# Kernel tuning notes

Measured on AMD Instinct MI355X. Metric: run time of the kernel, lower is better.

Reference implementation:

```python
import jax, jax.numpy as jnp
import numpy as np

M, NQ, NK, DX, H, HD, DT, KH = 2, 1024, 1024, 512, 8, 64, 2, 32
SCALE = HD ** -0.5


def setup_inputs() -> dict:
    key = jax.random.key(0)
    ks = jax.random.split(key, 12)
    w = lambda k, shape: jax.random.normal(k, shape, jnp.float32) * 0.02
    return dict(
        xq=jax.random.normal(ks[0], (M, NQ, DX), jnp.float32),
        xk=jax.random.normal(ks[1], (M, NK, DX), jnp.float32),
        xv=jax.random.normal(ks[2], (M, NK, DX), jnp.float32),
        tq=jax.random.normal(ks[3], (M, NQ, DT), jnp.float32),
        tk=jax.random.normal(ks[4], (M, NK, DT), jnp.float32),
        Wq=w(ks[5], (DX, H * HD)),
        Wk=w(ks[6], (DX, H * HD)),
        Wv=w(ks[7], (DX, H * HD)),
        Wo=w(ks[8], (H * HD, DX)),
        bo=jnp.zeros((DX,), jnp.float32),
        K1=w(ks[9], (DT, KH)),
        kb1=jnp.zeros((KH,), jnp.float32),
        K2=w(ks[10], (KH, H)),
        kb2=jnp.zeros((H,), jnp.float32),
    )


def _heads(t):
    # [b, n, h*d] -> [b, h, n, d]
    b, n, _ = t.shape
    return t.reshape(b, n, H, HD).transpose(0, 2, 1, 3)


def reference(xq, xk, xv, tq, tk, Wq, Wk, Wv, Wo, bo, K1, kb1, K2, kb2):
    q = _heads(xq @ Wq)            # [m,h,nq,d]
    k = _heads(xk @ Wk)            # [m,h,nk,d]
    token_dots = jnp.einsum('bhqd,bhkd->bhqk', q, k) * SCALE
    # diagonal attention term: query attends to its own (key/value-projected) token
    xq_k = _heads(xq @ Wk)
    diag_dots = jnp.sum(q * xq_k, axis=-1, keepdims=True) * SCALE   # [m,h,nq,1]
    token_dots = jnp.concatenate([token_dots, diag_dots], axis=-1)  # [m,h,nq,nk+1]
    # translation group action: pairwise differences, plus zero diagonal diff
    diff = tq[:, :, None, :] - tk[:, None, :, :]                    # [m,nq,nk,dt]
    diff = jnp.concatenate([diff, jnp.zeros((M, NQ, 1, DT), diff.dtype)], axis=2)
    # kernel network (MLP) -> per-head relative-position bias [m,nq,nk+1,h]
    kd = jax.nn.relu(diff @ K1 + kb1) @ K2 + kb2
    dots = token_dots + kd.transpose(0, 3, 1, 2)                    # [m,h,nq,nk+1]
    attn = jax.nn.softmax(dots, axis=-1)
    v = _heads(xv @ Wv)
    xq_v = _heads(xq @ Wv)
    out = jnp.einsum('bhqk,bhkd->bhqd', attn[..., :-1], v) + attn[..., -1:] * xq_v
    out = out.transpose(0, 2, 1, 3).reshape(M, NQ, H * HD) @ Wo + bo
    # phi_t is None -> tq_new = tq
    return (out, tq)
```

## Files before the change

kernel.cpp:

```cpp
#include <hip/hip_runtime.h>
#include <hip/hip_bf16.h>
#include <cstddef>

typedef __attribute__((ext_vector_type(8))) short bf16x8;
typedef __attribute__((ext_vector_type(4))) float f32x4;

constexpr int NH  = 8;
constexpr int HHD = 512;
constexpr int KHC = 32;
constexpr float SCALE_F = 0.125f;
constexpr int KSPLIT = 2;

__device__ __forceinline__ unsigned short f2bf(float f) {
    unsigned int u = __builtin_bit_cast(unsigned int, f);
    u = (u + 0x7FFFu + ((u >> 16) & 1u)) >> 16;
    return (unsigned short)u;
}
__device__ __forceinline__ float bf2f(unsigned short h) {
    unsigned int u = ((unsigned int)h) << 16;
    return __builtin_bit_cast(float, u);
}
__device__ __forceinline__ unsigned int cvt_pk_bf16(float lo, float hi) {
    unsigned int r;
    asm("v_cvt_pk_bf16_f32 %0, %1, %2" : "=v"(r) : "v"(lo), "v"(hi));
    return r;
}

struct Cast3 { const float* s[3]; unsigned short* d[3]; };
__global__ __launch_bounds__(256) void cast_x(Cast3 c) {
    const int z = blockIdx.z;
    const size_t i8 = ((size_t)blockIdx.x * 256 + threadIdx.x) * 8;
    const float4 f0 = *(const float4*)(c.s[z] + i8);
    const float4 f1 = *(const float4*)(c.s[z] + i8 + 4);
    ushort4 o0, o1;
    o0.x = f2bf(f0.x); o0.y = f2bf(f0.y); o0.z = f2bf(f0.z); o0.w = f2bf(f0.w);
    o1.x = f2bf(f1.x); o1.y = f2bf(f1.y); o1.z = f2bf(f1.z); o1.w = f2bf(f1.w);
    *(ushort4*)(c.d[z] + i8) = o0;
    *(ushort4*)(c.d[z] + i8 + 4) = o1;
}

struct Cast4 { const float* s[4]; unsigned short* d[4]; };
__global__ __launch_bounds__(256) void cast_wt(Cast4 c) {
    __shared__ unsigned short Ts[64][66];
    const int z = blockIdx.z;
    const float* W = c.s[z];
    unsigned short* Wt = c.d[z];
    const int t = threadIdx.x;
    const int k0 = blockIdx.x * 64, j0 = blockIdx.y * 64;

    {
        const int kr = t >> 2;
        const int jc = (t & 3) * 16;
        const float* g = W + (size_t)(k0 + kr) * 512 + j0 + jc;
        #pragma unroll
        for (int i4 = 0; i4 < 4; ++i4) {
            float4 f = *(const float4*)(g + i4 * 4);
            Ts[kr][jc + i4 * 4 + 0] = f2bf(f.x);
            Ts[kr][jc + i4 * 4 + 1] = f2bf(f.y);
            Ts[kr][jc + i4 * 4 + 2] = f2bf(f.z);
            Ts[kr][jc + i4 * 4 + 3] = f2bf(f.w);
        }
    }
    __syncthreads();
    {
        const int j = t >> 2;
        const int kseg = (t & 3) * 16;
        unsigned short tmp[16];
        #pragma unroll
        for (int i = 0; i < 16; ++i) tmp[i] = Ts[kseg + i][j];
        unsigned short* g = Wt + (size_t)(j0 + j) * 512 + k0 + kseg;
        #pragma unroll
        for (int i4 = 0; i4 < 4; ++i4)
            *(ushort4*)(g + i4 * 4) = *(ushort4*)&tmp[i4 * 4];
    }
}

__device__ __forceinline__ void mfma_gemm_core(const unsigned short* __restrict__ A,
                                               const unsigned short* __restrict__ Bt,
                                               int r0, int c0, f32x4 acc[2][4])
{
    __shared__ __align__(16) char As[16384];
    __shared__ __align__(16) char Bs[8192];

    const int tid = threadIdx.x;
    const int l = tid & 63, w = tid >> 6;
    const int lw = l & 15, lg = l >> 4;

    #pragma unroll
    for (int r = 0; r < 2; ++r)
        #pragma unroll
        for (int cb = 0; cb < 4; ++cb) acc[r][cb] = (f32x4){0.f, 0.f, 0.f, 0.f};

    const int arow_s = tid >> 1;
    const int ahalf  = tid & 1;
    const int brow_s = tid >> 2;
    const int bseg   = tid & 3;

    for (int kb = 0; kb < 512; kb += 64) {
        __syncthreads();
        {
            const unsigned short* g = A + (size_t)(r0 + arow_s) * 512 + kb + ahalf * 32;
            const int base = arow_s * 128 + ahalf * 64;
            const int sw = (arow_s & 7) << 4;
            #pragma unroll
            for (int i = 0; i < 4; ++i)
                *(float4*)(As + ((base + i * 16) ^ sw)) = *(const float4*)(g + i * 8);
        }
        {
            const unsigned short* g = Bt + (size_t)(c0 + brow_s) * 512 + kb + bseg * 16;
            const int base = brow_s * 128 + bseg * 32;
            const int sw = (brow_s & 7) << 4;
            #pragma unroll
            for (int i = 0; i < 2; ++i)
                *(float4*)(Bs + ((base + i * 16) ^ sw)) = *(const float4*)(g + i * 8);
        }
        __syncthreads();

        bf16x8 bfrag[4][2];
        #pragma unroll
        for (int cb = 0; cb < 4; ++cb) {
            const int bcol = cb * 16 + lw;
            const int sw = (bcol & 7) << 4;
            bfrag[cb][0] = *(const bf16x8*)(Bs + ((bcol * 128 + lg * 16) ^ sw));
            bfrag[cb][1] = *(const bf16x8*)(Bs + ((bcol * 128 + 64 + lg * 16) ^ sw));
        }
        #pragma unroll
        for (int r = 0; r < 2; ++r) {
            const int arow = w * 32 + r * 16 + lw;
            const int sw = (arow & 7) << 4;
            bf16x8 a0 = *(const bf16x8*)(As + ((arow * 128 + lg * 16) ^ sw));
            bf16x8 a1 = *(const bf16x8*)(As + ((arow * 128 + 64 + lg * 16) ^ sw));
            #pragma unroll
            for (int cb = 0; cb < 4; ++cb) {
                acc[r][cb] = __builtin_amdgcn_mfma_f32_16x16x32_bf16(a0, bfrag[cb][0], acc[r][cb], 0, 0, 0);
                acc[r][cb] = __builtin_amdgcn_mfma_f32_16x16x32_bf16(a1, bfrag[cb][1], acc[r][cb], 0, 0, 0);
            }
        }
    }
}

struct Proj5 {
    const unsigned short* A[5];
    const unsigned short* B[5];
    unsigned short* O[5];
    unsigned short* VT;
};

__global__ __launch_bounds__(256) void proj_mfma(Proj5 p) {
    const int z = blockIdx.z;
    const int r0 = blockIdx.x * 128, c0 = blockIdx.y * 64;
    f32x4 acc[2][4];
    mfma_gemm_core(p.A[z], p.B[z], r0, c0, acc);

    const int l = threadIdx.x & 63, w = threadIdx.x >> 6;
    const int lw = l & 15, lg = l >> 4;
    #pragma unroll
    for (int r = 0; r < 2; ++r)
        #pragma unroll
        for (int cb = 0; cb < 4; ++cb) {
            const int gc = c0 + cb * 16 + lw;
            const int h = gc >> 6, d = gc & 63;
            #pragma unroll
            for (int rr = 0; rr < 4; ++rr) {
                const int gr = r0 + w * 32 + r * 16 + lg * 4 + rr;
                const int m = gr >> 10, n = gr & 1023;
                const unsigned short v = f2bf(acc[r][cb][rr]);
                if (z == 2)
                    p.VT[(((size_t)m * NH + h) * 64 + d) * 1024 + n] = v;
                else
                    p.O[z][(((size_t)m * NH + h) * 1024 + n) * 64 + d] = v;
            }
        }
}

__global__ __launch_bounds__(256) void outproj_mfma(const unsigned short* __restrict__ A,
                                                    const unsigned short* __restrict__ Bt,
                                                    const float* __restrict__ bias,
                                                    float* __restrict__ C) {
    const int r0 = blockIdx.x * 128, c0 = blockIdx.y * 64;
    f32x4 acc[2][4];
    mfma_gemm_core(A, Bt, r0, c0, acc);

    const int l = threadIdx.x & 63, w = threadIdx.x >> 6;
    const int lw = l & 15, lg = l >> 4;
    #pragma unroll
    for (int r = 0; r < 2; ++r)
        #pragma unroll
        for (int cb = 0; cb < 4; ++cb) {
            const int gc = c0 + cb * 16 + lw;
            const float bv = bias[gc];
            #pragma unroll
            for (int rr = 0; rr < 4; ++rr) {
                const int gr = r0 + w * 32 + r * 16 + lg * 4 + rr;
                C[(size_t)gr * HHD + gc] = acc[r][cb][rr] + bv;
            }
        }
}

__global__ __launch_bounds__(256) void prep_k(const float* __restrict__ tq,
                                              const float* __restrict__ tk,
                                              const float* __restrict__ K1,
                                              const float* __restrict__ kb1,
                                              float* __restrict__ Aout,
                                              float* __restrict__ Bout)
{
    const int idx = blockIdx.x * 256 + threadIdx.x;
    const int which = idx >> 16;
    const int e = idx & 65535;
    const int row = e >> 5;
    const int j = e & 31;
    const float* t = which ? tk : tq;
    float v = t[row * 2 + 0] * K1[j] + t[row * 2 + 1] * K1[KHC + j];
    if (!which) v += kb1[j];
    (which ? Bout : Aout)[e] = v;
}

__global__ __launch_bounds__(256) void bias_mfma(const float* __restrict__ Aa,
                                                 const float* __restrict__ Bb,
                                                 const float* __restrict__ K2,
                                                 const float* __restrict__ kb2,
                                                 unsigned short* __restrict__ kd)
{
    const int tid = threadIdx.x;
    const int l = tid & 63;
    const int kb = tid >> 6;
    const int lw = l & 15, lg = l >> 4;
    const int bid = blockIdx.x;
    const int kt = bid & 15;
    const int qg = (bid >> 4) & 63;
    const int m  = bid >> 10;

    float k2f[8];
    #pragma unroll
    for (int e = 0; e < 8; ++e)
        k2f[e] = (lw < 8) ? K2[(lg * 8 + e) * 8 + lw] : 0.f;
    union { unsigned int u[4]; bf16x8 v; } bu;
    #pragma unroll
    for (int i = 0; i < 4; ++i) bu.u[i] = cvt_pk_bf16(k2f[2 * i], k2f[2 * i + 1]);
    const bf16x8 bfrag = bu.v;

    const float c0 = (lw < 8) ? kb2[lw] : 0.f;
    const f32x4 cini = {c0, c0, c0, c0};

    const int kglob = kt * 64 + kb * 16 + lw;
    const float* bp = Bb + ((size_t)m * 1024 + kglob) * 32 + lg * 8;
    const float4 b0 = *(const float4*)bp;
    const float4 b1 = *(const float4*)(bp + 4);
    const float bl[8] = {b0.x, b0.y, b0.z, b0.w, b1.x, b1.y, b1.z, b1.w};

    const float* arow = Aa + ((size_t)m * 1024 + qg * 16) * 32 + lg * 8;
    unsigned short* kout = kd + (size_t)(m * 8 + lw) * 1048576
                         + qg * 16384 + kt * 1024 + kb * 256 + lg * 64;

    #pragma unroll
    for (int t = 0; t < 16; t += 2) {
        const float4 a00 = *(const float4*)(arow + (size_t)t * 32);
        const float4 a01 = *(const float4*)(arow + (size_t)t * 32 + 4);
        union { unsigned int u[4]; bf16x8 v; } r0u;
        r0u.u[0] = cvt_pk_bf16(fmaxf(a00.x - bl[0], 0.f), fmaxf(a00.y - bl[1], 0.f));
        r0u.u[1] = cvt_pk_bf16(fmaxf(a00.z - bl[2], 0.f), fmaxf(a00.w - bl[3], 0.f));
        r0u.u[2] = cvt_pk_bf16(fmaxf(a01.x - bl[4], 0.f), fmaxf(a01.y - bl[5], 0.f));
        r0u.u[3] = cvt_pk_bf16(fmaxf(a01.z - bl[6], 0.f), fmaxf(a01.w - bl[7], 0.f));
        const f32x4 d0 = __builtin_amdgcn_mfma_f32_16x16x32_bf16(r0u.v, bfrag, cini, 0, 0, 0);

        const float4 a10 = *(const float4*)(arow + (size_t)(t + 1) * 32);
        const float4 a11 = *(const float4*)(arow + (size_t)(t + 1) * 32 + 4);
        union { unsigned int u[4]; bf16x8 v; } r1u;
        r1u.u[0] = cvt_pk_bf16(fmaxf(a10.x - bl[0], 0.f), fmaxf(a10.y - bl[1], 0.f));
        r1u.u[1] = cvt_pk_bf16(fmaxf(a10.z - bl[2], 0.f), fmaxf(a10.w - bl[3], 0.f));
        r1u.u[2] = cvt_pk_bf16(fmaxf(a11.x - bl[4], 0.f), fmaxf(a11.y - bl[5], 0.f));
        r1u.u[3] = cvt_pk_bf16(fmaxf(a11.z - bl[6], 0.f), fmaxf(a11.w - bl[7], 0.f));
        const f32x4 d1 = __builtin_amdgcn_mfma_f32_16x16x32_bf16(r1u.v, bfrag, cini, 0, 0, 0);

        if (lw < 8) {
            uint4 o;
            o.x = cvt_pk_bf16(d0[0], d0[1]);
            o.y = cvt_pk_bf16(d0[2], d0[3]);
            o.z = cvt_pk_bf16(d1[0], d1[1]);
            o.w = cvt_pk_bf16(d1[2], d1[3]);
            *(uint4*)(kout + t * 4) = o;
        }
    }
}

__global__ __launch_bounds__(256) void attn_mfma(
    const unsigned short* __restrict__ qh, const unsigned short* __restrict__ kh,
    const unsigned short* __restrict__ vt, const unsigned short* __restrict__ kd,
    float* __restrict__ pacc, float* __restrict__ pl)
{
    __shared__ __align__(16) char Ksh[8192];
    __shared__ __align__(16) char Vsh[8192];
    __shared__ __align__(16) char Psh[4][2048];

    const int tid = threadIdx.x;
    const int l = tid & 63;
    const int w = tid >> 6;
    const int lw = l & 15, lg = l >> 4;
    const int qt = blockIdx.x;
    const int mh = blockIdx.y;
    const int ks = blockIdx.z;
    const int q0 = qt * 64;

    const int qrow = q0 + w * 16 + lw;
    const unsigned short* qp = qh + ((size_t)mh * 1024 + qrow) * 64;
    const bf16x8 qf0 = *(const bf16x8*)(qp + lg * 8);
    const bf16x8 qf1 = *(const bf16x8*)(qp + 32 + lg * 8);

    f32x4 oacc[4] = {{0.f,0.f,0.f,0.f},{0.f,0.f,0.f,0.f},
                     {0.f,0.f,0.f,0.f},{0.f,0.f,0.f,0.f}};
    float lsum = 0.f;

    const int srow = tid >> 2;
    const int scol = (tid & 3) * 32;
    const int ssw  = (srow & 7) << 4;

    char* pbase = Psh[w];
    const int prsw = (lw & 7) << 4;
    const size_t kdwave = (((size_t)mh * 64 + qt * 4 + w) * 16 + ks * 8) * 1024;

    for (int kt = 0; kt < 8; ++kt) {
        const int k0 = ks * 512 + kt * 64;
        __syncthreads();
        {
            const char* g = (const char*)(kh + ((size_t)mh * 1024 + k0 + srow) * 64) + scol;
            const int a = srow * 128 + scol;
            *(float4*)(Ksh + (a ^ ssw))        = *(const float4*)g;
            *(float4*)(Ksh + ((a + 16) ^ ssw)) = *(const float4*)(g + 16);
        }
        {
            const char* g = (const char*)(vt + ((size_t)mh * 64 + srow) * 1024 + k0) + scol;
            const int a = srow * 128 + scol;
            *(float4*)(Vsh + (a ^ ssw))        = *(const float4*)g;
            *(float4*)(Vsh + ((a + 16) ^ ssw)) = *(const float4*)(g + 16);
        }
        __syncthreads();

        const unsigned short* kdt = kd + kdwave + (size_t)kt * 1024;
        #pragma unroll
        for (int kb = 0; kb < 4; ++kb) {
            f32x4 s = {0.f, 0.f, 0.f, 0.f};
            const int row = kb * 16 + lw;
            const int rsw = (row & 7) << 4;
            const int a0 = row * 128 + lg * 16;
            bf16x8 af0 = *(const bf16x8*)(Ksh + (a0 ^ rsw));
            s = __builtin_amdgcn_mfma_f32_16x16x32_bf16(af0, qf0, s, 0, 0, 0);
            bf16x8 af1 = *(const bf16x8*)(Ksh + ((a0 + 64) ^ rsw));
            s = __builtin_amdgcn_mfma_f32_16x16x32_bf16(af1, qf1, s, 0, 0, 0);

            ushort4 bb = *(const ushort4*)(kdt + kb * 256 + l * 4);
            float p0 = __expf(fmaf(s[0], SCALE_F, bf2f(bb.x)));
            float p1 = __expf(fmaf(s[1], SCALE_F, bf2f(bb.y)));
            float p2 = __expf(fmaf(s[2], SCALE_F, bf2f(bb.z)));
            float p3 = __expf(fmaf(s[3], SCALE_F, bf2f(bb.w)));
            lsum += (p0 + p1) + (p2 + p3);

            unsigned int u0 = f2bf(p0) | ((unsigned int)f2bf(p1) << 16);
            unsigned int u1 = f2bf(p2) | ((unsigned int)f2bf(p3) << 16);
            const int pa = lw * 128 + kb * 32 + lg * 8;
            *(uint2*)(pbase + (pa ^ prsw)) = make_uint2(u0, u1);
        }

        #pragma unroll
        for (int kc = 0; kc < 2; ++kc) {
            const int pa = lw * 128 + kc * 64 + lg * 16;
            bf16x8 pfrag = *(const bf16x8*)(pbase + (pa ^ prsw));
            #pragma unroll
            for (int db = 0; db < 4; ++db) {
                const int vrow = db * 16 + lw;
                const int va = vrow * 128 + kc * 64 + lg * 16;
                bf16x8 vfrag = *(const bf16x8*)(Vsh + (va ^ ((vrow & 7) << 4)));
                oacc[db] = __builtin_amdgcn_mfma_f32_16x16x32_bf16(pfrag, vfrag, oacc[db], 0, 0, 0);
            }
        }
    }

    lsum += __shfl_xor(lsum, 16, 64);
    lsum += __shfl_xor(lsum, 32, 64);

    float* pr = pacc + (((size_t)mh * KSPLIT + ks) * 1024) * 64;
    #pragma unroll
    for (int r = 0; r < 4; ++r) {
        const int qo = q0 + w * 16 + lg * 4 + r;
        float* rowp = pr + (size_t)qo * 64 + lw;
        rowp[0]  = oacc[0][r];
        rowp[16] = oacc[1][r];
        rowp[32] = oacc[2][r];
        rowp[48] = oacc[3][r];
    }
    if (lg == 0)
        pl[((size_t)mh * KSPLIT + ks) * 1024 + q0 + w * 16 + lw] = lsum;
}

__global__ __launch_bounds__(256) void reduce_k(
    const float* __restrict__ pacc, const float* __restrict__ pl,
    const unsigned short* __restrict__ qg, const unsigned short* __restrict__ xqk,
    const unsigned short* __restrict__ xqv, const float* __restrict__ K2,
    const float* __restrict__ kb1, const float* __restrict__ kb2,
    unsigned short* __restrict__ attn_out)
{
    const int rowid = blockIdx.x * 4 + (threadIdx.x >> 6);
    const int d = threadIdx.x & 63;
    const int mh = rowid >> 10;
    const int q = rowid & 1023;
    const int m = mh >> 3;
    const int h = mh & 7;

    float accsum = 0.f, lsumv = 0.f;
    #pragma unroll
    for (int kc = 0; kc < KSPLIT; ++kc) {
        accsum += pacc[(((size_t)mh * KSPLIT + kc) * 1024 + q) * 64 + d];
        lsumv  += pl[((size_t)mh * KSPLIT + kc) * 1024 + q];
    }
    const size_t ro = ((size_t)mh * 1024 + q) * 64 + d;
    float s = bf2f(qg[ro]) * bf2f(xqk[ro]);
    #pragma unroll
    for (int off = 32; off > 0; off >>= 1) s += __shfl_xor(s, off, 64);
    float bias_d = kb2[h];
    #pragma unroll
    for (int j = 0; j < KHC; ++j) bias_d += fmaxf(kb1[j], 0.f) * K2[j * NH + h];
    const float pd = __expf(fmaf(s, SCALE_F, bias_d));
    const float outv = (accsum + pd * bf2f(xqv[ro])) / (lsumv + pd);
    attn_out[((size_t)(m * 1024 + q)) * HHD + h * 64 + d] = f2bf(outv);
}

extern "C" void kernel_launch(void* const* d_in, const int* in_sizes, int n_in,
                              void* d_out, int out_size, void* d_ws, size_t ws_size,
                              hipStream_t stream)
{
    const float* xq  = (const float*)d_in[0];
    const float* xk  = (const float*)d_in[1];
    const float* xv  = (const float*)d_in[2];
    const float* tq  = (const float*)d_in[3];
    const float* tk  = (const float*)d_in[4];
    const float* Wq  = (const float*)d_in[5];
    const float* Wk  = (const float*)d_in[6];
    const float* Wv  = (const float*)d_in[7];
    const float* Wo  = (const float*)d_in[8];
    const float* bo  = (const float*)d_in[9];
    const float* K1  = (const float*)d_in[10];
    const float* kb1 = (const float*)d_in[11];
    const float* K2  = (const float*)d_in[12];
    const float* kb2 = (const float*)d_in[13];

    char* ws = (char*)d_ws;
    unsigned short* qh   = (unsigned short*)(ws);
    unsigned short* kh   = (unsigned short*)(ws +  2097152);
    unsigned short* vtp  = (unsigned short*)(ws +  4194304);
    unsigned short* xqk  = (unsigned short*)(ws +  6291456);
    unsigned short* xqv  = (unsigned short*)(ws +  8388608);
    float*          Aa   = (float*)(ws + 10485760);
    float*          Bb   = (float*)(ws + 10747904);
    unsigned short* kd   = (unsigned short*)(ws + 11010048);
    float*          pacc = (float*)(ws + 44564480);
    float*          pl   = (float*)(ws + 52953088);
    unsigned short* Wot  = (unsigned short*)(ws + 53084160);
    unsigned short* xa   = (unsigned short*)(ws + 11010048);
    unsigned short* xb   = (unsigned short*)(ws + 13107200);
    unsigned short* xc   = (unsigned short*)(ws + 15204352);
    unsigned short* Wqt  = (unsigned short*)(ws + 17301504);
    unsigned short* Wkt  = (unsigned short*)(ws + 17825792);
    unsigned short* Wvt  = (unsigned short*)(ws + 18350080);
    unsigned short* aout = (unsigned short*)(ws + 11010048);
    float*          outp = (float*)d_out;

    Cast3 c3; c3.s[0] = xq; c3.s[1] = xk; c3.s[2] = xv;
    c3.d[0] = xa; c3.d[1] = xb; c3.d[2] = xc;
    hipLaunchKernelGGL(cast_x, dim3(512, 1, 3), dim3(256), 0, stream, c3);
    Cast4 c4; c4.s[0] = Wq; c4.s[1] = Wk; c4.s[2] = Wv; c4.s[3] = Wo;
    c4.d[0] = Wqt; c4.d[1] = Wkt; c4.d[2] = Wvt; c4.d[3] = Wot;
    hipLaunchKernelGGL(cast_wt, dim3(8, 8, 4), dim3(256), 0, stream, c4);

    Proj5 p;
    p.A[0] = xa; p.B[0] = Wqt; p.O[0] = qh;
    p.A[1] = xb; p.B[1] = Wkt; p.O[1] = kh;
    p.A[2] = xc; p.B[2] = Wvt; p.O[2] = nullptr;
    p.A[3] = xa; p.B[3] = Wkt; p.O[3] = xqk;
    p.A[4] = xa; p.B[4] = Wvt; p.O[4] = xqv;
    p.VT = vtp;
    hipLaunchKernelGGL(proj_mfma, dim3(16, 8, 5), dim3(256), 0, stream, p);

    hipLaunchKernelGGL(prep_k, dim3(512), dim3(256), 0, stream, tq, tk, K1, kb1, Aa, Bb);

    hipLaunchKernelGGL(bias_mfma, dim3(2048), dim3(256), 0, stream, Aa, Bb, K2, kb2, kd);

    hipLaunchKernelGGL(attn_mfma, dim3(16, 16, KSPLIT), dim3(256), 0, stream,
                       qh, kh, vtp, kd, pacc, pl);

    hipLaunchKernelGGL(reduce_k, dim3(4096), dim3(256), 0, stream,
                       pacc, pl, qh, xqk, xqv, K2, kb1, kb2, aout);

    hipLaunchKernelGGL(outproj_mfma, dim3(16, 8, 1), dim3(256), 0, stream, aout, Wot, bo, outp);

    hipMemcpyAsync(outp + 1048576, tq, 4096 * sizeof(float),
                   hipMemcpyDeviceToDevice, stream);
}
```

Baseline: 164.7 us.

## Merge prep kernels into one launch and raise attention key split to four

Folds the three preparation kernels (activation cast, weight cast-transpose, kernel-MLP first layer) into a single launch that dispatches on block index, removing two kernel launches. Raises the attention key-split from 2 to 4 so the attention grid doubles to 1024 blocks with shorter loops, and adds a launch-bounds occupancy hint. The partial-accumulator buffer grows, so the workspace offsets are moved, and the reduction kernel must now combine more partials.

```diff
diff --git a/kernel.cpp b/kernel.cpp
--- a/kernel.cpp
+++ b/kernel.cpp
@@ -9,7 +9,7 @@
 constexpr int HHD = 512;
 constexpr int KHC = 32;
 constexpr float SCALE_F = 0.125f;
-constexpr int KSPLIT = 2;
+constexpr int KSPLIT = 4;
 
 __device__ __forceinline__ unsigned short f2bf(float f) {
     unsigned int u = __builtin_bit_cast(unsigned int, f);
@@ -26,52 +26,70 @@
     return r;
 }
 
-struct Cast3 { const float* s[3]; unsigned short* d[3]; };
-__global__ __launch_bounds__(256) void cast_x(Cast3 c) {
-    const int z = blockIdx.z;
-    const size_t i8 = ((size_t)blockIdx.x * 256 + threadIdx.x) * 8;
-    const float4 f0 = *(const float4*)(c.s[z] + i8);
-    const float4 f1 = *(const float4*)(c.s[z] + i8 + 4);
-    ushort4 o0, o1;
-    o0.x = f2bf(f0.x); o0.y = f2bf(f0.y); o0.z = f2bf(f0.z); o0.w = f2bf(f0.w);
-    o1.x = f2bf(f1.x); o1.y = f2bf(f1.y); o1.z = f2bf(f1.z); o1.w = f2bf(f1.w);
-    *(ushort4*)(c.d[z] + i8) = o0;
-    *(ushort4*)(c.d[z] + i8 + 4) = o1;
-}
-
-struct Cast4 { const float* s[4]; unsigned short* d[4]; };
-__global__ __launch_bounds__(256) void cast_wt(Cast4 c) {
+struct PrepAll {
+    const float* xs[3]; unsigned short* xd[3];
+    const float* wsrc[4]; unsigned short* wdst[4];
+    const float* tq; const float* tk;
+    const float* K1; const float* kb1;
+    float* Aa; float* Bb;
+};
+__global__ __launch_bounds__(256) void prep_all(PrepAll c) {
     __shared__ unsigned short Ts[64][66];
-    const int z = blockIdx.z;
-    const float* W = c.s[z];
-    unsigned short* Wt = c.d[z];
+    const int b = blockIdx.x;
     const int t = threadIdx.x;
-    const int k0 = blockIdx.x * 64, j0 = blockIdx.y * 64;
-
-    {
-        const int kr = t >> 2;
-        const int jc = (t & 3) * 16;
-        const float* g = W + (size_t)(k0 + kr) * 512 + j0 + jc;
-        #pragma unroll
-        for (int i4 = 0; i4 < 4; ++i4) {
-            float4 f = *(const float4*)(g + i4 * 4);
-            Ts[kr][jc + i4 * 4 + 0] = f2bf(f.x);
-            Ts[kr][jc + i4 * 4 + 1] = f2bf(f.y);
-            Ts[kr][jc + i4 * 4 + 2] = f2bf(f.z);
-            Ts[kr][jc + i4 * 4 + 3] = f2bf(f.w);
-        }
-    }
-    __syncthreads();
-    {
-        const int j = t >> 2;
-        const int kseg = (t & 3) * 16;
-        unsigned short tmp[16];
-        #pragma unroll
-        for (int i = 0; i < 16; ++i) tmp[i] = Ts[kseg + i][j];
-        unsigned short* g = Wt + (size_t)(j0 + j) * 512 + k0 + kseg;
-        #pragma unroll
-        for (int i4 = 0; i4 < 4; ++i4)
-            *(ushort4*)(g + i4 * 4) = *(ushort4*)&tmp[i4 * 4];
+
+    if (b < 1536) {
+        const int z = b / 512;
+        const size_t i8 = ((size_t)(b - z * 512) * 256 + t) * 8;
+        const float4 f0 = *(const float4*)(c.xs[z] + i8);
+        const float4 f1 = *(const float4*)(c.xs[z] + i8 + 4);
+        ushort4 o0, o1;
+        o0.x = f2bf(f0.x); o0.y = f2bf(f0.y); o0.z = f2bf(f0.z); o0.w = f2bf(f0.w);
+        o1.x = f2bf(f1.x); o1.y = f2bf(f1.y); o1.z = f2bf(f1.z); o1.w = f2bf(f1.w);
+        *(ushort4*)(c.xd[z] + i8) = o0;
+        *(ushort4*)(c.xd[z] + i8 + 4) = o1;
+    } else if (b < 1792) {
+        const int bb = b - 1536;
+        const int z = bb >> 6;
+        const int rem = bb & 63;
+        const int k0 = (rem & 7) * 64, j0 = (rem >> 3) * 64;
+        const float* W = c.wsrc[z];
+        unsigned short* Wt = c.wdst[z];
+        {
+            const int kr = t >> 2;
+            const int jc = (t & 3) * 16;
+            const float* g = W + (size_t)(k0 + kr) * 512 + j0 + jc;
+            #pragma unroll
+            for (int i4 = 0; i4 < 4; ++i4) {
+                float4 f = *(const float4*)(g + i4 * 4);
+                Ts[kr][jc + i4 * 4 + 0] = f2bf(f.x);
+                Ts[kr][jc + i4 * 4 + 1] = f2bf(f.y);
+                Ts[kr][jc + i4 * 4 + 2] = f2bf(f.z);
+                Ts[kr][jc + i4 * 4 + 3] = f2bf(f.w);
+            }
+        }
+        __syncthreads();
+        {
+            const int j = t >> 2;
+            const int kseg = (t & 3) * 16;
+            unsigned short tmp[16];
+            #pragma unroll
+            for (int i = 0; i < 16; ++i) tmp[i] = Ts[kseg + i][j];
+            unsigned short* g = Wt + (size_t)(j0 + j) * 512 + k0 + kseg;
+            #pragma unroll
+            for (int i4 = 0; i4 < 4; ++i4)
+                *(ushort4*)(g + i4 * 4) = *(ushort4*)&tmp[i4 * 4];
+        }
+    } else {
+        const int idx = (b - 1792) * 256 + t;
+        const int which = idx >> 16;
+        const int e = idx & 65535;
+        const int row = e >> 5;
+        const int j = e & 31;
+        const float* tt = which ? c.tk : c.tq;
+        float v = tt[row * 2 + 0] * c.K1[j] + tt[row * 2 + 1] * c.K1[KHC + j];
+        if (!which) v += c.kb1[j];
+        (which ? c.Bb : c.Aa)[e] = v;
     }
 }
 
@@ -195,24 +213,6 @@
                 C[(size_t)gr * HHD + gc] = acc[r][cb][rr] + bv;
             }
         }
-}
-
-__global__ __launch_bounds__(256) void prep_k(const float* __restrict__ tq,
-                                              const float* __restrict__ tk,
-                                              const float* __restrict__ K1,
-                                              const float* __restrict__ kb1,
-                                              float* __restrict__ Aout,
-                                              float* __restrict__ Bout)
-{
-    const int idx = blockIdx.x * 256 + threadIdx.x;
-    const int which = idx >> 16;
-    const int e = idx & 65535;
-    const int row = e >> 5;
-    const int j = e & 31;
-    const float* t = which ? tk : tq;
-    float v = t[row * 2 + 0] * K1[j] + t[row * 2 + 1] * K1[KHC + j];
-    if (!which) v += kb1[j];
-    (which ? Bout : Aout)[e] = v;
 }
 
 __global__ __launch_bounds__(256) void bias_mfma(const float* __restrict__ Aa,
@@ -283,7 +283,7 @@
     }
 }
 
-__global__ __launch_bounds__(256) void attn_mfma(
+__global__ __launch_bounds__(256, 4) void attn_mfma(
     const unsigned short* __restrict__ qh, const unsigned short* __restrict__ kh,
     const unsigned short* __restrict__ vt, const unsigned short* __restrict__ kd,
     float* __restrict__ pacc, float* __restrict__ pl)
@@ -316,10 +316,10 @@
 
     char* pbase = Psh[w];
     const int prsw = (lw & 7) << 4;
-    const size_t kdwave = (((size_t)mh * 64 + qt * 4 + w) * 16 + ks * 8) * 1024;
-
-    for (int kt = 0; kt < 8; ++kt) {
-        const int k0 = ks * 512 + kt * 64;
+    const size_t kdwave = (((size_t)mh * 64 + qt * 4 + w) * 16 + ks * 4) * 1024;
+
+    for (int kt = 0; kt < 4; ++kt) {
+        const int k0 = ks * 256 + kt * 64;
         __syncthreads();
         {
             const char* g = (const char*)(kh + ((size_t)mh * 1024 + k0 + srow) * 64) + scol;
@@ -452,8 +452,8 @@
     float*          Bb   = (float*)(ws + 10747904);
     unsigned short* kd   = (unsigned short*)(ws + 11010048);
     float*          pacc = (float*)(ws + 44564480);
-    float*          pl   = (float*)(ws + 52953088);
-    unsigned short* Wot  = (unsigned short*)(ws + 53084160);
+    float*          pl   = (float*)(ws + 61341696);
+    unsigned short* Wot  = (unsigned short*)(ws + 61603840);
     unsigned short* xa   = (unsigned short*)(ws + 11010048);
     unsigned short* xb   = (unsigned short*)(ws + 13107200);
     unsigned short* xc   = (unsigned short*)(ws + 15204352);
@@ -463,12 +463,13 @@
     unsigned short* aout = (unsigned short*)(ws + 11010048);
     float*          outp = (float*)d_out;
 
-    Cast3 c3; c3.s[0] = xq; c3.s[1] = xk; c3.s[2] = xv;
-    c3.d[0] = xa; c3.d[1] = xb; c3.d[2] = xc;
-    hipLaunchKernelGGL(cast_x, dim3(512, 1, 3), dim3(256), 0, stream, c3);
-    Cast4 c4; c4.s[0] = Wq; c4.s[1] = Wk; c4.s[2] = Wv; c4.s[3] = Wo;
-    c4.d[0] = Wqt; c4.d[1] = Wkt; c4.d[2] = Wvt; c4.d[3] = Wot;
-    hipLaunchKernelGGL(cast_wt, dim3(8, 8, 4), dim3(256), 0, stream, c4);
+    PrepAll pa;
+    pa.xs[0] = xq; pa.xs[1] = xk; pa.xs[2] = xv;
+    pa.xd[0] = xa; pa.xd[1] = xb; pa.xd[2] = xc;
+    pa.wsrc[0] = Wq; pa.wsrc[1] = Wk; pa.wsrc[2] = Wv; pa.wsrc[3] = Wo;
+    pa.wdst[0] = Wqt; pa.wdst[1] = Wkt; pa.wdst[2] = Wvt; pa.wdst[3] = Wot;
+    pa.tq = tq; pa.tk = tk; pa.K1 = K1; pa.kb1 = kb1; pa.Aa = Aa; pa.Bb = Bb;
+    hipLaunchKernelGGL(prep_all, dim3(2304), dim3(256), 0, stream, pa);
 
     Proj5 p;
     p.A[0] = xa; p.B[0] = Wqt; p.O[0] = qh;
@@ -479,8 +480,6 @@
     p.VT = vtp;
     hipLaunchKernelGGL(proj_mfma, dim3(16, 8, 5), dim3(256), 0, stream, p);
 
-    hipLaunchKernelGGL(prep_k, dim3(512), dim3(256), 0, stream, tq, tk, K1, kb1, Aa, Bb);
-
     hipLaunchKernelGGL(bias_mfma, dim3(2048), dim3(256), 0, stream, Aa, Bb, K2, kb2, kd);
 
     hipLaunchKernelGGL(attn_mfma, dim3(16, 16, KSPLIT), dim3(256), 0, stream,
```

Result: faster. 160.6 us (-2.5%).
